# Optimization experiments

Hardware: AMD Instinct MI355X
Metric: run time of the kernel (lower is better)

## Reference

```python
import jax, jax.numpy as jnp
import numpy as np

HID, E, S, L_CAP, EPS = 768, 1536, 128, 512, 1e-5


def _rope_seq(x):
    """RoPE along axis 1. x: [b, n, 2, s]."""
    n, s = x.shape[1], x.shape[-1]
    half = s // 2
    inv_freq = jnp.power(10000.0, -jnp.arange(half, dtype=x.dtype) / half)  # [half]
    sinusoid = jnp.arange(n, dtype=x.dtype)[:, None, None] * inv_freq       # [n,1,half]
    sin, cos = jnp.sin(sinusoid), jnp.cos(sinusoid)
    x1, x2 = jnp.split(x, 2, axis=-1)
    return jnp.concatenate([x1 * cos - x2 * sin, x2 * cos + x1 * sin], axis=-1)


def setup_inputs() -> dict:
    key = jax.random.key(0)
    ks = jax.random.split(key, 6)
    B, L = 32, 512
    return {
        "x": jax.random.normal(ks[0], (B, L, HID), dtype=jnp.float32),
        "ln_gamma": jnp.ones((HID,), jnp.float32),
        "ln_beta": jnp.zeros((HID,), jnp.float32),
        "uv_W": jax.random.normal(ks[1], (HID, 2 * E + S), jnp.float32) * 0.02,
        "uv_b": jnp.zeros((2 * E + S,), jnp.float32),
        "gamma_qk": jax.random.normal(ks[2], (2, S), jnp.float32) * 0.02,
        "beta_qk": jnp.zeros((2, S), jnp.float32),
        "w_rel": jax.random.normal(ks[3], (2 * L_CAP - 1,), jnp.float32) * 0.02,
        "o_W": jax.random.normal(ks[4], (E, HID), jnp.float32) * 0.02,
        "o_b": jnp.zeros((HID,), jnp.float32),
    }


def reference(x, ln_gamma, ln_beta, uv_W, uv_b, gamma_qk, beta_qk, w_rel, o_W, o_b):
    L = x.shape[1]
    shortcut = x
    # LayerNorm
    mu = jnp.mean(x, axis=-1, keepdims=True)
    var = jnp.mean(jnp.square(x - mu), axis=-1, keepdims=True)
    xn = (x - mu) * jax.lax.rsqrt(var + EPS) * ln_gamma + ln_beta
    # uv projection + silu, split into u, v, base
    uv = jax.nn.silu(xn @ uv_W + uv_b)                       # [b, n, 2e+s]
    u, v, base = jnp.split(uv, [E, 2 * E], axis=-1)          # [b,n,e], [b,n,e], [b,n,s]
    # per-head affine then RoPE -> q, k
    base = base[..., None, :] * gamma_qk + beta_qk           # [b, n, 2, s]
    base = _rope_seq(base)
    q, k = base[..., 0, :], base[..., 1, :]
    # relu^2 attention kernel with Toeplitz relative position bias
    qk = jnp.einsum('bnd,bmd->bnm', q, k)
    idx = jnp.arange(L)
    bias = w_rel[idx[None, :] - idx[:, None] + L - 1]        # bias[i,j] = w[j-i+L-1]
    kernel = jnp.square(jax.nn.relu(qk / L + bias))
    # gated value aggregation + output projection + residual
    out = u * jnp.einsum('bnm,bme->bne', kernel, v)
    out = out @ o_W + o_b
    return out + shortcut
```

## Files before the change

### kernel.cpp

```cpp
#include <hip/hip_runtime.h>
#include <hip/hip_bf16.h>
#include <math.h>

typedef __bf16 bf16x8 __attribute__((ext_vector_type(8)));
typedef float f32x4 __attribute__((ext_vector_type(4)));
typedef unsigned short u16x4 __attribute__((ext_vector_type(4)));

__device__ __forceinline__ float b2f(unsigned short h) {
    unsigned int u = ((unsigned int)h) << 16;
    return __builtin_bit_cast(float, u);
}
__device__ __forceinline__ unsigned short f2b(float f) {
    unsigned int u = __builtin_bit_cast(unsigned int, f);
    u += 0x7FFFu + ((u >> 16) & 1u);
    return (unsigned short)(u >> 16);
}
__device__ __forceinline__ float silu(float c) {
    return c * __builtin_amdgcn_rcpf(1.0f + __expf(-c));
}

__global__ __launch_bounds__(256) void k_convT(const float* __restrict__ src,
                                               unsigned short* __restrict__ dst,
                                               int R, int C) {
    __shared__ float tile[32][33];
    int tx = threadIdx.x, ty = threadIdx.y;
    int r0 = blockIdx.y << 5, c0 = blockIdx.x << 5;
#pragma unroll
    for (int i = 0; i < 4; ++i)
        tile[ty + 8 * i][tx] = src[(long long)(r0 + ty + 8 * i) * C + c0 + tx];
    __syncthreads();
#pragma unroll
    for (int i = 0; i < 4; ++i)
        dst[(long long)(c0 + ty + 8 * i) * R + r0 + tx] = f2b(tile[tx][ty + 8 * i]);
}

__global__ __launch_bounds__(256) void k_ln(const float* __restrict__ x,
                                            const float* __restrict__ g,
                                            const float* __restrict__ b,
                                            unsigned short* __restrict__ xn) {
    int row = blockIdx.x;
    int t = threadIdx.x;
    const float* xr = x + (long long)row * 768;
    float v0 = xr[t], v1 = xr[t + 256], v2 = xr[t + 512];
    float s = v0 + v1 + v2;
    float q = v0 * v0 + v1 * v1 + v2 * v2;
#pragma unroll
    for (int off = 32; off > 0; off >>= 1) {
        s += __shfl_xor(s, off);
        q += __shfl_xor(q, off);
    }
    __shared__ float ss[4], sq[4];
    int w = t >> 6;
    if ((t & 63) == 0) { ss[w] = s; sq[w] = q; }
    __syncthreads();
    float S_ = ss[0] + ss[1] + ss[2] + ss[3];
    float Q_ = sq[0] + sq[1] + sq[2] + sq[3];
    float mu = S_ * (1.0f / 768.0f);
    float var = Q_ * (1.0f / 768.0f) - mu * mu;
    float rs = rsqrtf(var + 1e-5f);
    unsigned short* xo = xn + (long long)row * 768;
    xo[t]       = f2b((v0 - mu) * rs * g[t]       + b[t]);
    xo[t + 256] = f2b((v1 - mu) * rs * g[t + 256] + b[t + 256]);
    xo[t + 512] = f2b((v2 - mu) * rs * g[t + 512] + b[t + 512]);
}

__global__ __launch_bounds__(128) void k_rope(const unsigned short* __restrict__ bS,
                                              const float* __restrict__ gqk,
                                              const float* __restrict__ bqk,
                                              unsigned short* __restrict__ q,
                                              unsigned short* __restrict__ k) {
    int row = blockIdx.x;
    int l = row & 511;
    int s = threadIdx.x;
    int j = s & 63;
    int partner = s ^ 64;
    float b0 = b2f(bS[(long long)row * 128 + s]);
    float bp = b2f(bS[(long long)row * 128 + partner]);
    float invf = __expf((float)j * -0.14391156831f);
    float th = (float)l * invf;
    float sn, cs;
    __sincosf(th, &sn, &cs);
    float sign = (s < 64) ? -1.0f : 1.0f;
    float preq  = b0 * gqk[s]           + bqk[s];
    float preqp = bp * gqk[partner]     + bqk[partner];
    q[(long long)row * 128 + s] = f2b(preq * cs + sign * preqp * sn);
    float prek  = b0 * gqk[128 + s]       + bqk[128 + s];
    float prekp = bp * gqk[128 + partner] + bqk[128 + partner];
    k[(long long)row * 128 + s] = f2b(prek * cs + sign * prekp * sn);
}

template <int EPI, bool SWAP, bool SWZ>
__global__ __launch_bounds__(256) void k_gemm(const unsigned short* __restrict__ A,
                                              const unsigned short* __restrict__ B,
                                              int K, long long strideA, long long strideB,
                                              void* p0, const void* p1, const void* p2,
                                              const void* p3) {
    __shared__ __align__(16) unsigned short As[128 * 64];
    __shared__ __align__(16) unsigned short Bs[128 * 64];
    int t = threadIdx.x;
    int w = t >> 6, lane = t & 63;
    int wr = w >> 1, wc = w & 1;
    int bx = blockIdx.x, by = blockIdx.y, bz = blockIdx.z;
    if constexpr (SWZ) {
        int gx = gridDim.x;
        int nb = gx * gridDim.y;
        int bid = by * gx + bx;
        int s = (bid & 7) * (nb >> 3) + (bid >> 3);
        bx = s % gx;
        by = s / gx;
    }
    const unsigned short* Ab = A + bz * strideA + (long long)by * 128 * K;
    const unsigned short* Bb = B + bz * strideB + (long long)bx * 128 * K;

    f32x4 acc[4][4];
#pragma unroll
    for (int m = 0; m < 4; ++m)
#pragma unroll
        for (int n = 0; n < 4; ++n) acc[m][n] = (f32x4){0.f, 0.f, 0.f, 0.f};

    int rowA = (w << 3) + (lane >> 3);
    int colA = (lane & 7) << 3;

    for (int k0 = 0; k0 < K; k0 += 64) {
#pragma unroll
        for (int i = 0; i < 4; ++i) {
            int r = (i << 5) + rowA;
            __builtin_amdgcn_global_load_lds(
                (const __attribute__((address_space(1))) void*)(Ab + (long long)r * K + k0 + colA),
                (__attribute__((address_space(3))) void*)(&As[(i << 11) + (w << 9)]),
                16, 0, 0);
            __builtin_amdgcn_global_load_lds(
                (const __attribute__((address_space(1))) void*)(Bb + (long long)r * K + k0 + colA),
                (__attribute__((address_space(3))) void*)(&Bs[(i << 11) + (w << 9)]),
                16, 0, 0);
        }
        __syncthreads();
#pragma unroll
        for (int ks = 0; ks < 2; ++ks) {
            bf16x8 af[4], bfr[4];
#pragma unroll
            for (int m = 0; m < 4; ++m)
                af[m] = *(const bf16x8*)&As[((wr << 6) + (m << 4) + (lane & 15)) * 64 +
                                            (ks << 5) + ((lane >> 4) << 3)];
#pragma unroll
            for (int n = 0; n < 4; ++n)
                bfr[n] = *(const bf16x8*)&Bs[((wc << 6) + (n << 4) + (lane & 15)) * 64 +
                                             (ks << 5) + ((lane >> 4) << 3)];
#pragma unroll
            for (int m = 0; m < 4; ++m)
#pragma unroll
                for (int n = 0; n < 4; ++n) {
                    if constexpr (SWAP)
                        acc[m][n] = __builtin_amdgcn_mfma_f32_16x16x32_bf16(bfr[n], af[m],
                                                                            acc[m][n], 0, 0, 0);
                    else
                        acc[m][n] = __builtin_amdgcn_mfma_f32_16x16x32_bf16(af[m], bfr[n],
                                                                            acc[m][n], 0, 0, 0);
                }
        }
        __syncthreads();
    }

    int c15 = lane & 15, qq = lane >> 4;
    int rowb = (by << 7) + (wr << 6) + c15;
    int colb = (bx << 7) + (wc << 6) + (qq << 2);
#pragma unroll
    for (int m = 0; m < 4; ++m) {
#pragma unroll
        for (int n = 0; n < 4; ++n) {
            int grow = rowb + (m << 4);
            int gcol = colb + (n << 4);
            f32x4 a = acc[m][n];
            if constexpr (EPI == 5) {
                f32x4 bb = *(const f32x4*)((const float*)p3 + gcol);
                u16x4 o;
#pragma unroll
                for (int i = 0; i < 4; ++i) o[i] = f2b(silu(a[i] + bb[i]));
                *(u16x4*)((unsigned short*)p0 + (long long)grow * 128 + gcol) = o;
            } else {
                const float* wrel = (const float*)p1;
                int base = gcol - grow + 511;
                u16x4 o;
#pragma unroll
                for (int i = 0; i < 4; ++i) {
                    float val = a[i] * (1.0f / 512.0f) + wrel[base + i];
                    val = fmaxf(val, 0.0f);
                    o[i] = f2b(val * val);
                }
                *(u16x4*)((unsigned short*)p0 +
                          ((long long)(bz * 512 + grow)) * 512 + gcol) = o;
            }
        }
    }
}

#define AS1P const __attribute__((address_space(1))) void*
#define AS3P __attribute__((address_space(3))) void*

__device__ __forceinline__ void stage64(const unsigned short* __restrict__ g, long long ldk,
                                        unsigned short* lds, int r0, int w, int lane) {
    int row = r0 + (w << 3) + (lane >> 3);
    int colb = (lane & 7) << 4;
    int scolb = colb ^ ((row & 7) << 4);
    __builtin_amdgcn_global_load_lds(
        (AS1P)((const char*)g + (long long)row * (ldk * 2) + scolb),
        (AS3P)((char*)lds + (r0 << 7) + (w << 10)), 16, 0, 0);
}
__device__ __forceinline__ const bf16x8* frag_ptr(const unsigned short* tile, int row, int colb) {
    return (const bf16x8*)((const char*)tile + (row << 7) + (colb ^ ((row & 7) << 4)));
}

template <int EPI, bool SWAP, bool SWZ>
__global__ __launch_bounds__(512, 2) void k_gemm8(const unsigned short* __restrict__ A,
                                                  const unsigned short* __restrict__ B,
                                                  int K, long long strideA, long long strideB,
                                                  void* p0, const void* p1, const void* p2,
                                                  const void* p3) {
    __shared__ __align__(16) unsigned short As[2][256 * 64];
    __shared__ __align__(16) unsigned short Bs[2][256 * 64];
    int t = threadIdx.x;
    int w = t >> 6, lane = t & 63;
    int wr = w >> 2, wc = w & 3;
    int c15 = lane & 15, qq = lane >> 4;
    int bx = blockIdx.x, by = blockIdx.y, bz = blockIdx.z;
    if constexpr (SWZ) {
        int gx = gridDim.x;
        int nb = gx * gridDim.y;
        int bid = by * gx + bx;
        int s = (bid & 7) * (nb >> 3) + (bid >> 3);
        bx = s % gx;
        by = s / gx;
    }
    const unsigned short* Ab = A + bz * strideA + (long long)by * 256 * K;
    const unsigned short* Bb = B + bz * strideB + (long long)bx * 256 * K;

    f32x4 acc[8][4];
#pragma unroll
    for (int m = 0; m < 8; ++m)
#pragma unroll
        for (int n = 0; n < 4; ++n) acc[m][n] = (f32x4){0.f, 0.f, 0.f, 0.f};

#pragma unroll
    for (int h = 0; h < 4; ++h) {
        stage64(Ab, K, &As[0][0], h << 6, w, lane);
        stage64(Bb, K, &Bs[0][0], h << 6, w, lane);
    }
    asm volatile("s_waitcnt vmcnt(0)" ::: "memory");
    __builtin_amdgcn_s_barrier();

    const int NT = K >> 6;
    for (int kt = 0; kt < NT; ++kt) {
        const int cur = kt & 1;
        const unsigned short* At = &As[cur][0];
        const unsigned short* Bt = &Bs[cur][0];
        unsigned short* Asn = &As[cur ^ 1][0];
        unsigned short* Bsn = &Bs[cur ^ 1][0];
        const unsigned short* An = Ab + (long long)(kt + 1) * 64;
        const unsigned short* Bn = Bb + (long long)(kt + 1) * 64;
        const bool pf = (kt + 1 < NT);
        bf16x8 bfr[4][2], af[2][2];

#define LOAD_A(p)                                                                   \
    _Pragma("unroll") for (int j = 0; j < 2; ++j)                                   \
        _Pragma("unroll") for (int ks = 0; ks < 2; ++ks)                            \
            af[j][ks] = *frag_ptr(At, wr * 128 + (2 * (p) + j) * 16 + c15,          \
                                  ks * 64 + qq * 16);
#define DO_MFMA(p)                                                                  \
    __builtin_amdgcn_s_setprio(1);                                                  \
    _Pragma("unroll") for (int j = 0; j < 2; ++j)                                   \
        _Pragma("unroll") for (int n = 0; n < 4; ++n)                               \
            _Pragma("unroll") for (int ks = 0; ks < 2; ++ks) {                      \
                if constexpr (SWAP)                                                 \
                    acc[2 * (p) + j][n] = __builtin_amdgcn_mfma_f32_16x16x32_bf16(  \
                        bfr[n][ks], af[j][ks], acc[2 * (p) + j][n], 0, 0, 0);       \
                else                                                                \
                    acc[2 * (p) + j][n] = __builtin_amdgcn_mfma_f32_16x16x32_bf16(  \
                        af[j][ks], bfr[n][ks], acc[2 * (p) + j][n], 0, 0, 0);       \
            }                                                                       \
    __builtin_amdgcn_s_setprio(0);

#pragma unroll
        for (int n = 0; n < 4; ++n)
#pragma unroll
            for (int ks = 0; ks < 2; ++ks)
                bfr[n][ks] = *frag_ptr(Bt, wc * 64 + n * 16 + c15, ks * 64 + qq * 16);
        LOAD_A(0)
        if (pf) {
            stage64(An, K, Asn, 0, w, lane);
            stage64(An, K, Asn, 64, w, lane);
            stage64(An, K, Asn, 128, w, lane);
            stage64(An, K, Asn, 192, w, lane);
        }
        __builtin_amdgcn_s_barrier();
        asm volatile("s_waitcnt lgkmcnt(0)" ::: "memory");
        DO_MFMA(0)
        __builtin_amdgcn_s_barrier();
        LOAD_A(1)
        if (pf) {
            stage64(Bn, K, Bsn, 0, w, lane);
            stage64(Bn, K, Bsn, 64, w, lane);
        }
        __builtin_amdgcn_s_barrier();
        asm volatile("s_waitcnt lgkmcnt(0)" ::: "memory");
        DO_MFMA(1)
        __builtin_amdgcn_s_barrier();
        LOAD_A(2)
        if (pf) {
            stage64(Bn, K, Bsn, 128, w, lane);
            stage64(Bn, K, Bsn, 192, w, lane);
        }
        __builtin_amdgcn_s_barrier();
        asm volatile("s_waitcnt lgkmcnt(0)" ::: "memory");
        DO_MFMA(2)
        __builtin_amdgcn_s_barrier();
        LOAD_A(3)
        __builtin_amdgcn_s_barrier();
        asm volatile("s_waitcnt lgkmcnt(0)" ::: "memory");
        DO_MFMA(3)
        asm volatile("s_waitcnt vmcnt(0)" ::: "memory");
        __builtin_amdgcn_s_barrier();
#undef LOAD_A
#undef DO_MFMA
    }

    if constexpr (SWAP) {
        int rowb = by * 256 + wr * 128 + c15;
        int colb = bx * 256 + wc * 64 + (qq << 2);
#pragma unroll
        for (int m = 0; m < 8; ++m) {
#pragma unroll
            for (int n = 0; n < 4; ++n) {
                int R = rowb + m * 16;
                int C = colb + n * 16;
                f32x4 a = acc[m][n];
                if constexpr (EPI == 0) {
                    f32x4 bb = *(const f32x4*)((const float*)p3 + C);
                    u16x4 o;
#pragma unroll
                    for (int i = 0; i < 4; ++i) o[i] = f2b(silu(a[i] + bb[i]));
                    *(u16x4*)((unsigned short*)p0 + (long long)R * 1536 + C) = o;
                } else if constexpr (EPI == 2) {
                    long long idx = ((long long)(bz * 512 + R)) * 1536 + C;
                    u16x4 uu = *(const u16x4*)((const unsigned short*)p1 + idx);
                    u16x4 o;
#pragma unroll
                    for (int i = 0; i < 4; ++i) o[i] = f2b(a[i] * b2f(uu[i]));
                    *(u16x4*)((unsigned short*)p0 + idx) = o;
                } else {
                    long long idx = (long long)R * 768 + C;
                    f32x4 xv = *(const f32x4*)((const float*)p2 + idx);
                    f32x4 ob = *(const f32x4*)((const float*)p1 + C);
                    f32x4 o;
#pragma unroll
                    for (int i = 0; i < 4; ++i) o[i] = a[i] + ob[i] + xv[i];
                    *(f32x4*)((float*)p0 + idx) = o;
                }
            }
        }
    } else {
        int rowb = by * 256 + wr * 128 + (qq << 2);
        int colb = bx * 256 + wc * 64 + c15;
#pragma unroll
        for (int m = 0; m < 8; ++m) {
#pragma unroll
            for (int n = 0; n < 4; ++n) {
                int grow = rowb + m * 16;
                int e = colb + n * 16;
                float bias = ((const float*)p3)[1536 + e];
                f32x4 a = acc[m][n];
                u16x4 o;
#pragma unroll
                for (int i = 0; i < 4; ++i) o[i] = f2b(silu(a[i] + bias));
                int bb2 = grow >> 9, mm = grow & 511;
                *(u16x4*)((unsigned short*)p0 + ((long long)bb2 * 1536 + e) * 512 + mm) = o;
            }
        }
    }
}

extern "C" void kernel_launch(void* const* d_in, const int* in_sizes, int n_in,
                              void* d_out, int out_size, void* d_ws, size_t ws_size,
                              hipStream_t stream) {
    const float* x     = (const float*)d_in[0];
    const float* ln_g  = (const float*)d_in[1];
    const float* ln_b  = (const float*)d_in[2];
    const float* uv_W  = (const float*)d_in[3];
    const float* uv_b  = (const float*)d_in[4];
    const float* g_qk  = (const float*)d_in[5];
    const float* b_qk  = (const float*)d_in[6];
    const float* w_rel = (const float*)d_in[7];
    const float* o_W   = (const float*)d_in[8];
    const float* o_b   = (const float*)d_in[9];
    float* out = (float*)d_out;

    char* ws = (char*)d_ws;
    size_t off = 0;
    auto alloc = [&](size_t bytes) {
        void* p = ws + off;
        off += (bytes + 255) & ~(size_t)255;
        return p;
    };
    unsigned short* uvWT = (unsigned short*)alloc(3200ll * 768 * 2);
    unsigned short* oWT  = (unsigned short*)alloc(768ll * 1536 * 2);
    unsigned short* xn   = (unsigned short*)alloc(16384ll * 768 * 2);
    unsigned short* u    = (unsigned short*)alloc(16384ll * 1536 * 2);
    unsigned short* vT   = (unsigned short*)alloc(32ll * 1536 * 512 * 2);
    unsigned short* bS   = (unsigned short*)alloc(16384ll * 128 * 2);
    unsigned short* q    = (unsigned short*)alloc(32ll * 512 * 128 * 2);
    unsigned short* k    = (unsigned short*)alloc(32ll * 512 * 128 * 2);
    unsigned short* P     = xn;
    unsigned short* gated = u;

    k_convT<<<dim3(100, 24), dim3(32, 8), 0, stream>>>(uv_W, uvWT, 768, 3200);
    k_convT<<<dim3(24, 48), dim3(32, 8), 0, stream>>>(o_W, oWT, 1536, 768);
    k_ln<<<16384, 256, 0, stream>>>(x, ln_g, ln_b, xn);
    k_gemm8<0, true, true><<<dim3(6, 64), 512, 0, stream>>>(
        xn, uvWT, 768, 0, 0, (void*)u, nullptr, nullptr, (const void*)uv_b);
    k_gemm8<4, false, true><<<dim3(6, 64), 512, 0, stream>>>(
        xn, uvWT + 1536ll * 768, 768, 0, 0, (void*)vT, nullptr, nullptr, (const void*)uv_b);
    k_gemm<5, true, true><<<dim3(1, 128), 256, 0, stream>>>(
        xn, uvWT + 3072ll * 768, 768, 0, 0, (void*)bS, nullptr, nullptr,
        (const void*)(uv_b + 3072));
    k_rope<<<16384, 128, 0, stream>>>(bS, g_qk, b_qk, q, k);
    k_gemm<1, true, false><<<dim3(4, 4, 32), 256, 0, stream>>>(
        q, k, 128, 512ll * 128, 512ll * 128, (void*)P, (const void*)w_rel, nullptr, nullptr);
    k_gemm8<2, true, false><<<dim3(6, 2, 32), 512, 0, stream>>>(
        P, vT, 512, 512ll * 512, 1536ll * 512, (void*)gated, (const void*)u, nullptr, nullptr);
    k_gemm8<3, true, true><<<dim3(3, 64), 512, 0, stream>>>(
        gated, oWT, 1536, 0, 0, (void*)out, (const void*)o_b, (const void*)x, nullptr);
}
```

Measured before the change: 313.7 us.

## Replace double-buffered 256x256 GEMM with 4-stage K=32 pipelined kernel

```diff
diff --git a/kernel.cpp b/kernel.cpp
--- a/kernel.cpp
+++ b/kernel.cpp
@@ -5,6 +5,9 @@
 typedef __bf16 bf16x8 __attribute__((ext_vector_type(8)));
 typedef float f32x4 __attribute__((ext_vector_type(4)));
 typedef unsigned short u16x4 __attribute__((ext_vector_type(4)));
+
+#define AS1P const __attribute__((address_space(1))) void*
+#define AS3P __attribute__((address_space(3))) void*
 
 __device__ __forceinline__ float b2f(unsigned short h) {
     unsigned int u = ((unsigned int)h) << 16;
@@ -126,13 +129,11 @@
         for (int i = 0; i < 4; ++i) {
             int r = (i << 5) + rowA;
             __builtin_amdgcn_global_load_lds(
-                (const __attribute__((address_space(1))) void*)(Ab + (long long)r * K + k0 + colA),
-                (__attribute__((address_space(3))) void*)(&As[(i << 11) + (w << 9)]),
-                16, 0, 0);
+                (AS1P)(Ab + (long long)r * K + k0 + colA),
+                (AS3P)(&As[(i << 11) + (w << 9)]), 16, 0, 0);
             __builtin_amdgcn_global_load_lds(
-                (const __attribute__((address_space(1))) void*)(Bb + (long long)r * K + k0 + colA),
-                (__attribute__((address_space(3))) void*)(&Bs[(i << 11) + (w << 9)]),
-                16, 0, 0);
+                (AS1P)(Bb + (long long)r * K + k0 + colA),
+                (AS3P)(&Bs[(i << 11) + (w << 9)]), 16, 0, 0);
         }
         __syncthreads();
 #pragma unroll
@@ -194,30 +195,35 @@
     }
 }
 
-#define AS1P const __attribute__((address_space(1))) void*
-#define AS3P __attribute__((address_space(3))) void*
-
-__device__ __forceinline__ void stage64(const unsigned short* __restrict__ g, long long ldk,
-                                        unsigned short* lds, int r0, int w, int lane) {
-    int row = r0 + (w << 3) + (lane >> 3);
-    int colb = (lane & 7) << 4;
-    int scolb = colb ^ ((row & 7) << 4);
+__device__ __forceinline__ bf16x8 ldsread(const unsigned short* p) {
+    bf16x8 r;
+    unsigned int off =
+        (unsigned int)(unsigned long long)(__attribute__((address_space(3))) const void*)p;
+    asm volatile("ds_read_b128 %0, %1" : "=v"(r) : "v"(off));
+    return r;
+}
+
+__device__ __forceinline__ void stage_tile(const unsigned short* __restrict__ g, int ldk,
+                                           unsigned short* lds, int t) {
+    int row = t >> 2;
+    int colb = (t & 3) << 4;
     __builtin_amdgcn_global_load_lds(
-        (AS1P)((const char*)g + (long long)row * (ldk * 2) + scolb),
-        (AS3P)((char*)lds + (r0 << 7) + (w << 10)), 16, 0, 0);
-}
-__device__ __forceinline__ const bf16x8* frag_ptr(const unsigned short* tile, int row, int colb) {
-    return (const bf16x8*)((const char*)tile + (row << 7) + (colb ^ ((row & 7) << 4)));
-}
-
-template <int EPI, bool SWAP, bool SWZ>
-__global__ __launch_bounds__(512, 2) void k_gemm8(const unsigned short* __restrict__ A,
-                                                  const unsigned short* __restrict__ B,
-                                                  int K, long long strideA, long long strideB,
-                                                  void* p0, const void* p1, const void* p2,
-                                                  const void* p3) {
-    __shared__ __align__(16) unsigned short As[2][256 * 64];
-    __shared__ __align__(16) unsigned short Bs[2][256 * 64];
+        (AS1P)((const char*)(g + (long long)row * ldk) + colb),
+        (AS3P)((char*)lds + t * 16), 16, 0, 0);
+    __builtin_amdgcn_global_load_lds(
+        (AS1P)((const char*)(g + (long long)(row + 128) * ldk) + colb),
+        (AS3P)((char*)lds + 8192 + t * 16), 16, 0, 0);
+}
+
+template <int EPI, bool SWAP, bool SWZ, int NT>
+__global__ __launch_bounds__(512, 2) void k_pipe(const unsigned short* __restrict__ A,
+                                                 const unsigned short* __restrict__ B,
+                                                 long long strideA, long long strideB,
+                                                 void* p0, const void* p1, const void* p2,
+                                                 const void* p3) {
+    constexpr int K = NT * 32;
+    __shared__ __align__(16) unsigned short As[4][256 * 32];
+    __shared__ __align__(16) unsigned short Bs[4][256 * 32];
     int t = threadIdx.x;
     int w = t >> 6, lane = t & 63;
     int wr = w >> 2, wc = w & 3;
@@ -241,86 +247,48 @@
         for (int n = 0; n < 4; ++n) acc[m][n] = (f32x4){0.f, 0.f, 0.f, 0.f};
 
 #pragma unroll
-    for (int h = 0; h < 4; ++h) {
-        stage64(Ab, K, &As[0][0], h << 6, w, lane);
-        stage64(Bb, K, &Bs[0][0], h << 6, w, lane);
-    }
-    asm volatile("s_waitcnt vmcnt(0)" ::: "memory");
-    __builtin_amdgcn_s_barrier();
-
-    const int NT = K >> 6;
+    for (int p = 0; p < 3; ++p) {
+        stage_tile(Ab + p * 32, K, &As[p][0], t);
+        stage_tile(Bb + p * 32, K, &Bs[p][0], t);
+    }
+
     for (int kt = 0; kt < NT; ++kt) {
-        const int cur = kt & 1;
-        const unsigned short* At = &As[cur][0];
-        const unsigned short* Bt = &Bs[cur][0];
-        unsigned short* Asn = &As[cur ^ 1][0];
-        unsigned short* Bsn = &Bs[cur ^ 1][0];
-        const unsigned short* An = Ab + (long long)(kt + 1) * 64;
-        const unsigned short* Bn = Bb + (long long)(kt + 1) * 64;
-        const bool pf = (kt + 1 < NT);
-        bf16x8 bfr[4][2], af[2][2];
-
-#define LOAD_A(p)                                                                   \
-    _Pragma("unroll") for (int j = 0; j < 2; ++j)                                   \
-        _Pragma("unroll") for (int ks = 0; ks < 2; ++ks)                            \
-            af[j][ks] = *frag_ptr(At, wr * 128 + (2 * (p) + j) * 16 + c15,          \
-                                  ks * 64 + qq * 16);
-#define DO_MFMA(p)                                                                  \
-    __builtin_amdgcn_s_setprio(1);                                                  \
-    _Pragma("unroll") for (int j = 0; j < 2; ++j)                                   \
-        _Pragma("unroll") for (int n = 0; n < 4; ++n)                               \
-            _Pragma("unroll") for (int ks = 0; ks < 2; ++ks) {                      \
-                if constexpr (SWAP)                                                 \
-                    acc[2 * (p) + j][n] = __builtin_amdgcn_mfma_f32_16x16x32_bf16(  \
-                        bfr[n][ks], af[j][ks], acc[2 * (p) + j][n], 0, 0, 0);       \
-                else                                                                \
-                    acc[2 * (p) + j][n] = __builtin_amdgcn_mfma_f32_16x16x32_bf16(  \
-                        af[j][ks], bfr[n][ks], acc[2 * (p) + j][n], 0, 0, 0);       \
-            }                                                                       \
-    __builtin_amdgcn_s_setprio(0);
-
+        if (kt <= NT - 3)
+            asm volatile("s_waitcnt vmcnt(8)" ::: "memory");
+        else if (kt == NT - 2)
+            asm volatile("s_waitcnt vmcnt(4)" ::: "memory");
+        else
+            asm volatile("s_waitcnt vmcnt(0)" ::: "memory");
+        __builtin_amdgcn_s_barrier();
+        __builtin_amdgcn_sched_barrier(0);
+        if (kt + 3 < NT) {
+            stage_tile(Ab + (long long)(kt + 3) * 32, K, &As[(kt + 3) & 3][0], t);
+            stage_tile(Bb + (long long)(kt + 3) * 32, K, &Bs[(kt + 3) & 3][0], t);
+        }
+        const unsigned short* At = &As[kt & 3][0];
+        const unsigned short* Bt = &Bs[kt & 3][0];
+        bf16x8 bfr[4], af[8];
 #pragma unroll
         for (int n = 0; n < 4; ++n)
-#pragma unroll
-            for (int ks = 0; ks < 2; ++ks)
-                bfr[n][ks] = *frag_ptr(Bt, wc * 64 + n * 16 + c15, ks * 64 + qq * 16);
-        LOAD_A(0)
-        if (pf) {
-            stage64(An, K, Asn, 0, w, lane);
-            stage64(An, K, Asn, 64, w, lane);
-            stage64(An, K, Asn, 128, w, lane);
-            stage64(An, K, Asn, 192, w, lane);
-        }
-        __builtin_amdgcn_s_barrier();
+            bfr[n] = ldsread(Bt + ((wc << 6) + (n << 4) + c15) * 32 + (qq << 3));
+#pragma unroll
+        for (int m = 0; m < 8; ++m)
+            af[m] = ldsread(At + ((wr << 7) + (m << 4) + c15) * 32 + (qq << 3));
         asm volatile("s_waitcnt lgkmcnt(0)" ::: "memory");
-        DO_MFMA(0)
-        __builtin_amdgcn_s_barrier();
-        LOAD_A(1)
-        if (pf) {
-            stage64(Bn, K, Bsn, 0, w, lane);
-            stage64(Bn, K, Bsn, 64, w, lane);
-        }
-        __builtin_amdgcn_s_barrier();
-        asm volatile("s_waitcnt lgkmcnt(0)" ::: "memory");
-        DO_MFMA(1)
-        __builtin_amdgcn_s_barrier();
-        LOAD_A(2)
-        if (pf) {
-            stage64(Bn, K, Bsn, 128, w, lane);
-            stage64(Bn, K, Bsn, 192, w, lane);
-        }
-        __builtin_amdgcn_s_barrier();
-        asm volatile("s_waitcnt lgkmcnt(0)" ::: "memory");
-        DO_MFMA(2)
-        __builtin_amdgcn_s_barrier();
-        LOAD_A(3)
-        __builtin_amdgcn_s_barrier();
-        asm volatile("s_waitcnt lgkmcnt(0)" ::: "memory");
-        DO_MFMA(3)
-        asm volatile("s_waitcnt vmcnt(0)" ::: "memory");
-        __builtin_amdgcn_s_barrier();
-#undef LOAD_A
-#undef DO_MFMA
+        __builtin_amdgcn_sched_barrier(0);
+        __builtin_amdgcn_s_setprio(1);
+#pragma unroll
+        for (int m = 0; m < 8; ++m)
+#pragma unroll
+            for (int n = 0; n < 4; ++n) {
+                if constexpr (SWAP)
+                    acc[m][n] = __builtin_amdgcn_mfma_f32_16x16x32_bf16(bfr[n], af[m],
+                                                                        acc[m][n], 0, 0, 0);
+                else
+                    acc[m][n] = __builtin_amdgcn_mfma_f32_16x16x32_bf16(af[m], bfr[n],
+                                                                        acc[m][n], 0, 0, 0);
+            }
+        __builtin_amdgcn_s_setprio(0);
     }
 
     if constexpr (SWAP) {
@@ -414,18 +382,18 @@
     k_convT<<<dim3(100, 24), dim3(32, 8), 0, stream>>>(uv_W, uvWT, 768, 3200);
     k_convT<<<dim3(24, 48), dim3(32, 8), 0, stream>>>(o_W, oWT, 1536, 768);
     k_ln<<<16384, 256, 0, stream>>>(x, ln_g, ln_b, xn);
-    k_gemm8<0, true, true><<<dim3(6, 64), 512, 0, stream>>>(
-        xn, uvWT, 768, 0, 0, (void*)u, nullptr, nullptr, (const void*)uv_b);
-    k_gemm8<4, false, true><<<dim3(6, 64), 512, 0, stream>>>(
-        xn, uvWT + 1536ll * 768, 768, 0, 0, (void*)vT, nullptr, nullptr, (const void*)uv_b);
+    k_pipe<0, true, true, 24><<<dim3(6, 64), 512, 0, stream>>>(
+        xn, uvWT, 0, 0, (void*)u, nullptr, nullptr, (const void*)uv_b);
+    k_pipe<4, false, true, 24><<<dim3(6, 64), 512, 0, stream>>>(
+        xn, uvWT + 1536ll * 768, 0, 0, (void*)vT, nullptr, nullptr, (const void*)uv_b);
     k_gemm<5, true, true><<<dim3(1, 128), 256, 0, stream>>>(
         xn, uvWT + 3072ll * 768, 768, 0, 0, (void*)bS, nullptr, nullptr,
         (const void*)(uv_b + 3072));
     k_rope<<<16384, 128, 0, stream>>>(bS, g_qk, b_qk, q, k);
     k_gemm<1, true, false><<<dim3(4, 4, 32), 256, 0, stream>>>(
         q, k, 128, 512ll * 128, 512ll * 128, (void*)P, (const void*)w_rel, nullptr, nullptr);
-    k_gemm8<2, true, false><<<dim3(6, 2, 32), 512, 0, stream>>>(
-        P, vT, 512, 512ll * 512, 1536ll * 512, (void*)gated, (const void*)u, nullptr, nullptr);
-    k_gemm8<3, true, true><<<dim3(3, 64), 512, 0, stream>>>(
-        gated, oWT, 1536, 0, 0, (void*)out, (const void*)o_b, (const void*)x, nullptr);
-}
+    k_pipe<2, true, false, 16><<<dim3(6, 2, 32), 512, 0, stream>>>(
+        P, vT, 512ll * 512, 1536ll * 512, (void*)gated, (const void*)u, nullptr, nullptr);
+    k_pipe<3, true, true, 48><<<dim3(3, 64), 512, 0, stream>>>(
+        gated, oWT, 0, 0, (void*)out, (const void*)o_b, (const void*)x, nullptr);
+}
```

After: 326.6 us. +4.1%, slower.
